# Optimization experiments

Hardware: AMD Instinct MI355X
Metric: run time of the kernel (lower is better)

The kernel has to match this reference:

```python
import jax, jax.numpy as jnp
import numpy as np

B, N, D = 8, 2048, 1024
NEG = -1e9


def setup_inputs() -> dict:
    key = jax.random.key(0)
    kx, kl, kq, kk, kv, ko = jax.random.split(key, 6)
    x = jax.random.normal(kx, (B, N, D), dtype=jnp.float32)
    # prefix padding mask: each clip has a random valid length in [N//2, N]
    lengths = jax.random.randint(kl, (B,), N // 2, N + 1)
    mask = jnp.arange(N)[None, :] < lengths[:, None]  # [B, N] bool
    s = 1.0 / np.sqrt(D)
    Wq = jax.random.normal(kq, (D, D), dtype=jnp.float32) * s  # nn.Linear weight [out,in]
    Wk = jax.random.normal(kk, (D, D), dtype=jnp.float32) * s
    Wv = jax.random.normal(kv, (D, D), dtype=jnp.float32) * s
    Wo = jax.random.normal(ko, (D, D), dtype=jnp.float32) * s
    return {"x": x, "mask": mask, "Wq": Wq, "Wk": Wk, "Wv": Wv, "Wo": Wo}


def reference(x, mask, Wq, Wk, Wv, Wo):
    # Linear (no bias): y = x @ W.T
    K = jnp.einsum('bnd,ed->bne', x, Wk)
    Q = jnp.einsum('bnd,ed->bne', x, Wq) * 0.06
    V = jnp.einsum('bnd,ed->bne', x, Wv)
    logits = jnp.einsum('bne,bme->bnm', Q, K)  # [B, N, N]
    # attention_mask = outer product of padding mask (matmul of mask with its transpose)
    attn_mask = mask[:, :, None] & mask[:, None, :]
    logits = jnp.where(attn_mask, logits, NEG)
    att_weights = jax.nn.softmax(logits, axis=-1)
    # dropout (p=0.5) is identity in eval mode
    # y = (V^T @ W)^T  ->  y[b,i,:] = sum_j att[b,j,i] * V[b,j,:]
    y = jnp.einsum('bji,bjd->bid', att_weights, V)
    y = jnp.einsum('bid,ed->bie', y, Wo)
    return (y, att_weights)
```

## Files before the change

kernel.cpp:

```cpp
#include <hip/hip_runtime.h>
#include <math.h>

typedef __attribute__((ext_vector_type(8))) short short8;
typedef __attribute__((ext_vector_type(4))) float f32x4;

namespace {
constexpr int B_ = 8;
constexpr int N_ = 2048;
constexpr int D_ = 1024;
constexpr float NEGV = -1.0e9f;
}

__device__ __forceinline__ unsigned short f2bf(float x) {
    union { float f; unsigned u; } v; v.f = x;
    unsigned u = v.u + 0x7fffu + ((v.u >> 16) & 1u);
    return (unsigned short)(u >> 16);
}

__global__ __launch_bounds__(256)
void k_lengths(const unsigned char* __restrict__ mask, int* __restrict__ L)
{
    const int b = blockIdx.x;
    const int t = threadIdx.x;
    const bool u8 = (mask[1] != 0);
    int cnt = 0;
    if (u8) {
        for (int n = t; n < N_; n += 256)
            cnt += (mask[(size_t)b * N_ + n] != 0) ? 1 : 0;
    } else {
        const int* mi = (const int*)mask;
        for (int n = t; n < N_; n += 256)
            cnt += (mi[(size_t)b * N_ + n] != 0) ? 1 : 0;
    }
    __shared__ int red[256];
    red[t] = cnt;
    __syncthreads();
    for (int s = 128; s > 0; s >>= 1) {
        if (t < s) red[t] += red[t + s];
        __syncthreads();
    }
    if (t == 0) L[b] = red[0];
}

__global__ __launch_bounds__(256)
void convert_bf16(const float* __restrict__ in, unsigned short* __restrict__ out,
                  int n4, float alpha)
{
    const int i = blockIdx.x * 256 + threadIdx.x;
    if (i >= n4) return;
    const float4 v = ((const float4*)in)[i];
    ushort4 o;
    o.x = f2bf(v.x * alpha); o.y = f2bf(v.y * alpha);
    o.z = f2bf(v.z * alpha); o.w = f2bf(v.w * alpha);
    ((ushort4*)out)[i] = o;
}

template <int OUT_MODE>
__global__ __launch_bounds__(512, 2)
void gemm_nt_256(const unsigned short* __restrict__ A, int lda, long strideA,
                 const unsigned short* __restrict__ Bm, int ldb, long strideB,
                 void* __restrict__ Cout, int ldc, long strideC,
                 int K, const int* __restrict__ Lp)
{
    __shared__ __attribute__((aligned(16))) short As[2][8192];
    __shared__ __attribute__((aligned(16))) short Bs[2][8192];

    const int tid  = threadIdx.x;
    const int lane = tid & 63;
    const int wave = tid >> 6;
    const int wr   = wave >> 2;
    const int wc   = wave & 3;

    const unsigned gx   = gridDim.x;
    const unsigned gxy  = gx * gridDim.y;
    const unsigned total = gxy * gridDim.z;
    const unsigned orig = blockIdx.x + gx * blockIdx.y + gxy * blockIdx.z;
    unsigned wg = orig;
    if ((total & 7u) == 0u)
        wg = (orig & 7u) * (total >> 3) + (orig >> 3);
    const unsigned bz  = wg / gxy;
    const unsigned rem = wg - bz * gxy;
    const unsigned byy = rem / gx;
    const unsigned bxx = rem - byy * gx;

    const int b  = (int)bz;
    const int m0 = (int)byy * 256;
    const int n0 = (int)bxx * 256;

    int Lb = 0;
    if (OUT_MODE == 2) {
        Lb = Lp[b];
        if (m0 >= Lb) return;
        if (n0 >= Lb) {
            float* C = (float*)Cout + (long)b * strideC;
            const float4 nv = make_float4(NEGV, NEGV, NEGV, NEGV);
            const int rl = tid >> 6;
            const int c4 = (tid & 63) * 4;
#pragma unroll
            for (int l = 0; l < 32; ++l)
                *(float4*)(C + (long)(m0 + l * 8 + rl) * ldc + n0 + c4) = nv;
            return;
        }
    }

    const unsigned short* Ab = A  + (long)b * strideA;
    const unsigned short* Bb = Bm + (long)b * strideB;

    const int srow = tid >> 2;
    const int sseg = ((tid & 3) ^ ((tid >> 3) & 3)) * 8;
    const unsigned short* gA = Ab + (long)(m0 + srow) * lda + sseg;
    const unsigned short* gB = Bb + (long)(n0 + srow) * ldb + sseg;
    const int ldst = (tid & ~63) * 8;

    const int q  = lane >> 4, r = lane & 15;
    const int arb = (wr * 128 + r) * 32;
    const int brb = (wc * 64 + r) * 32;
    const int pk  = (q ^ ((r >> 1) & 3)) * 8;

    const int NT = K >> 5;

    short8 aQ[8];
    short8 bQ[4];
    f32x4  acc[8][4] = {};

#define STAGE_A(dd, kt) do {                                                   \
    __builtin_amdgcn_global_load_lds(                                          \
        (const __attribute__((address_space(1))) void*)(gA + (long)(kt)*32),   \
        (__attribute__((address_space(3))) void*)(&As[dd][ldst]), 16, 0, 0);   \
    __builtin_amdgcn_global_load_lds(                                          \
        (const __attribute__((address_space(1))) void*)(gA + (long)128*lda + (long)(kt)*32), \
        (__attribute__((address_space(3))) void*)(&As[dd][4096 + ldst]), 16, 0, 0);          \
} while (0)

#define STAGE_B(dd, kt) do {                                                   \
    __builtin_amdgcn_global_load_lds(                                          \
        (const __attribute__((address_space(1))) void*)(gB + (long)(kt)*32),   \
        (__attribute__((address_space(3))) void*)(&Bs[dd][ldst]), 16, 0, 0);   \
    __builtin_amdgcn_global_load_lds(                                          \
        (const __attribute__((address_space(1))) void*)(gB + (long)128*ldb + (long)(kt)*32), \
        (__attribute__((address_space(3))) void*)(&Bs[dd][4096 + ldst]), 16, 0, 0);          \
} while (0)

#define RD_A(dd) do {                                                          \
    _Pragma("unroll") for (int mr_ = 0; mr_ < 8; ++mr_)                        \
        aQ[mr_] = *(const short8*)&As[dd][arb + mr_ * 512 + pk];               \
} while (0)

#define RD_B(dd, nh) do {                                                      \
    bQ[(nh)*2 + 0] = *(const short8*)&Bs[dd][brb + ((nh)*2 + 0) * 512 + pk];   \
    bQ[(nh)*2 + 1] = *(const short8*)&Bs[dd][brb + ((nh)*2 + 1) * 512 + pk];   \
} while (0)

#define BARX __builtin_amdgcn_s_barrier()
#define WAIT_LGKM0 do { asm volatile("s_waitcnt lgkmcnt(0)" ::: "memory"); \
                        __builtin_amdgcn_sched_barrier(0); } while (0)
#define WAIT_VM0   do { asm volatile("s_waitcnt vmcnt(0)"   ::: "memory"); \
                        __builtin_amdgcn_sched_barrier(0); } while (0)
#define WAIT_VM2   do { asm volatile("s_waitcnt vmcnt(2)"   ::: "memory"); \
                        __builtin_amdgcn_sched_barrier(0); } while (0)

#define MFMA_PH(nh) do {                                                       \
    __builtin_amdgcn_s_setprio(1);                                             \
    _Pragma("unroll") for (int mr_ = 0; mr_ < 8; ++mr_)                        \
    _Pragma("unroll") for (int nr_ = 0; nr_ < 2; ++nr_)                        \
        acc[mr_][(nh)*2 + nr_] = __builtin_amdgcn_mfma_f32_16x16x32_bf16(      \
            aQ[mr_], bQ[(nh)*2 + nr_], acc[mr_][(nh)*2 + nr_], 0, 0, 0);       \
    __builtin_amdgcn_s_setprio(0);                                             \
} while (0)

#define TILE_STEP(d, kt) do {                                                  \
                                                                       \
    RD_A(d); RD_B(d, 0);                                                       \
    if ((kt) + 1 < NT) STAGE_B((d) ^ 1, (kt) + 1);                             \
    BARX; WAIT_LGKM0; MFMA_PH(0); BARX;                                        \
                                                                       \
    RD_B(d, 1);                                                                \
    if ((kt) + 2 < NT) { STAGE_A(d, (kt) + 2); WAIT_VM2; } else { WAIT_VM0; }  \
    BARX; WAIT_LGKM0; MFMA_PH(1); BARX;                                        \
} while (0)

    STAGE_A(0, 0); STAGE_B(0, 0); STAGE_A(1, 1);
    WAIT_VM2; BARX;

    for (int kt = 0; kt < NT; kt += 2) {
        TILE_STEP(0, kt);
        TILE_STEP(1, kt + 1);
    }

#undef STAGE_A
#undef STAGE_B
#undef RD_A
#undef RD_B
#undef BARX
#undef WAIT_LGKM0
#undef WAIT_VM0
#undef WAIT_VM2
#undef MFMA_PH
#undef TILE_STEP

    const int rbase = m0 + wr * 128;
    const int cbase = n0 + wc * 64;
    if (OUT_MODE == 1) {
        unsigned short* C = (unsigned short*)Cout + (long)b * strideC;
#pragma unroll
        for (int mt = 0; mt < 8; ++mt)
#pragma unroll
            for (int nt = 0; nt < 4; ++nt)
#pragma unroll
                for (int rr = 0; rr < 4; ++rr) {
                    const int grow = rbase + mt * 16 + q * 4 + rr;
                    const int gcol = cbase + nt * 16 + r;
                    C[(long)grow * ldc + gcol] = f2bf(acc[mt][nt][rr]);
                }
    } else if (OUT_MODE == 0) {
        float* C = (float*)Cout + (long)b * strideC;
#pragma unroll
        for (int mt = 0; mt < 8; ++mt)
#pragma unroll
            for (int nt = 0; nt < 4; ++nt)
#pragma unroll
                for (int rr = 0; rr < 4; ++rr) {
                    const int grow = rbase + mt * 16 + q * 4 + rr;
                    const int gcol = cbase + nt * 16 + r;
                    C[(long)grow * ldc + gcol] = acc[mt][nt][rr];
                }
    } else {
        float* C = (float*)Cout + (long)b * strideC;
#pragma unroll
        for (int mt = 0; mt < 8; ++mt)
#pragma unroll
            for (int nt = 0; nt < 4; ++nt)
#pragma unroll
                for (int rr = 0; rr < 4; ++rr) {
                    const int grow = rbase + mt * 16 + q * 4 + rr;
                    const int gcol = cbase + nt * 16 + r;
                    const float val = (grow < Lb && gcol < Lb) ? acc[mt][nt][rr] : NEGV;
                    C[(long)grow * ldc + gcol] = val;
                }
    }
}

__global__ __launch_bounds__(256)
void softmax_rows(float* __restrict__ Att, const int* __restrict__ Lp)
{
    const size_t row = blockIdx.x;
    const int i = (int)(row & (N_ - 1));
    const int b = (int)(row >> 11);
    float* p = Att + row * (size_t)N_;
    const int t = threadIdx.x;

    if (i >= Lp[b]) {
        const float c = 1.0f / 2048.0f;
        const float4 cv = make_float4(c, c, c, c);
        *(float4*)(p + t * 4)        = cv;
        *(float4*)(p + 1024 + t * 4) = cv;
        return;
    }

    float4 v0 = *(float4*)(p + t * 4);
    float4 v1 = *(float4*)(p + 1024 + t * 4);

    float mx = fmaxf(fmaxf(fmaxf(v0.x, v0.y), fmaxf(v0.z, v0.w)),
                     fmaxf(fmaxf(v1.x, v1.y), fmaxf(v1.z, v1.w)));
#pragma unroll
    for (int o = 32; o > 0; o >>= 1) mx = fmaxf(mx, __shfl_xor(mx, o, 64));

    __shared__ float red[8];
    const int wv = t >> 6;
    if ((t & 63) == 0) red[wv] = mx;
    __syncthreads();
    mx = fmaxf(fmaxf(red[0], red[1]), fmaxf(red[2], red[3]));

    float e[8];
    e[0] = expf(v0.x - mx); e[1] = expf(v0.y - mx);
    e[2] = expf(v0.z - mx); e[3] = expf(v0.w - mx);
    e[4] = expf(v1.x - mx); e[5] = expf(v1.y - mx);
    e[6] = expf(v1.z - mx); e[7] = expf(v1.w - mx);
    float s = ((e[0] + e[1]) + (e[2] + e[3])) + ((e[4] + e[5]) + (e[6] + e[7]));
#pragma unroll
    for (int o = 32; o > 0; o >>= 1) s += __shfl_xor(s, o, 64);
    if ((t & 63) == 0) red[4 + wv] = s;
    __syncthreads();
    const float inv = 1.0f / (red[4] + red[5] + red[6] + red[7]);

    *(float4*)(p + t * 4)        = make_float4(e[0] * inv, e[1] * inv, e[2] * inv, e[3] * inv);
    *(float4*)(p + 1024 + t * 4) = make_float4(e[4] * inv, e[5] * inv, e[6] * inv, e[7] * inv);
}

__global__ __launch_bounds__(256)
void transpose_att_bf16(const float* __restrict__ att, unsigned short* __restrict__ attT)
{
    __shared__ float tile[64][65];
    const int b  = blockIdx.z;
    const int j0 = blockIdx.y * 64;
    const int i0 = blockIdx.x * 64;
    const float* src = att + (long)b * N_ * N_;
    unsigned short* dst = attT + (long)b * N_ * N_;
    const int t = threadIdx.x;
#pragma unroll
    for (int l = 0; l < 4; ++l) {
        const int idx = t + l * 256;
        const int jj = idx >> 4;
        const int i4 = (idx & 15) * 4;
        const float4 v = *(const float4*)(src + (long)(j0 + jj) * N_ + i0 + i4);
        tile[i4 + 0][jj] = v.x;
        tile[i4 + 1][jj] = v.y;
        tile[i4 + 2][jj] = v.z;
        tile[i4 + 3][jj] = v.w;
    }
    __syncthreads();
#pragma unroll
    for (int l = 0; l < 4; ++l) {
        const int idx = t + l * 256;
        const int ii = idx >> 4;
        const int j4 = (idx & 15) * 4;
        ushort4 o;
        o.x = f2bf(tile[ii][j4 + 0]);
        o.y = f2bf(tile[ii][j4 + 1]);
        o.z = f2bf(tile[ii][j4 + 2]);
        o.w = f2bf(tile[ii][j4 + 3]);
        *(ushort4*)(dst + (long)(i0 + ii) * N_ + j0 + j4) = o;
    }
}

__global__ __launch_bounds__(256)
void transpose_v_bf16(const unsigned short* __restrict__ qkv, unsigned short* __restrict__ vt)
{
    __shared__ unsigned short tile[64][68];
    const int j0 = blockIdx.x * 64;
    const int d0 = blockIdx.y * 64;
    const int t = threadIdx.x;
#pragma unroll
    for (int l = 0; l < 4; ++l) {
        const int idx = t + l * 256;
        const int jj = idx >> 4;
        const int d4 = (idx & 15) * 4;
        const ushort4 v = *(const ushort4*)(qkv + (long)(j0 + jj) * 3072 + 2048 + d0 + d4);
        tile[d4 + 0][jj] = v.x;
        tile[d4 + 1][jj] = v.y;
        tile[d4 + 2][jj] = v.z;
        tile[d4 + 3][jj] = v.w;
    }
    __syncthreads();
#pragma unroll
    for (int l = 0; l < 4; ++l) {
        const int idx = t + l * 256;
        const int dd = idx >> 4;
        const int j4 = (idx & 15) * 4;
        ushort4 o;
        o.x = tile[dd][j4 + 0];
        o.y = tile[dd][j4 + 1];
        o.z = tile[dd][j4 + 2];
        o.w = tile[dd][j4 + 3];
        *(ushort4*)(vt + (long)(d0 + dd) * 16384 + j0 + j4) = o;
    }
}

extern "C" void kernel_launch(void* const* d_in, const int* in_sizes, int n_in,
                              void* d_out, int out_size, void* d_ws, size_t ws_size,
                              hipStream_t stream)
{
    const float* x  = (const float*)d_in[0];
    const unsigned char* mask = (const unsigned char*)d_in[1];
    const float* Wq = (const float*)d_in[2];
    const float* Wk = (const float*)d_in[3];
    const float* Wv = (const float*)d_in[4];
    const float* Wo = (const float*)d_in[5];

    float* y   = (float*)d_out;
    float* att = (float*)d_out + (size_t)B_ * N_ * D_;

    char* ws = (char*)d_ws;
    int* L = (int*)ws;
    unsigned short* Wqkvb = (unsigned short*)(ws + 256);
    unsigned short* Wob   = Wqkvb + 3145728;
    unsigned short* xb    = Wob + 1048576;
    unsigned short* QKVb  = xb + 16777216;
    unsigned short* VT    = QKVb + 50331648;
    unsigned short* attT  = QKVb;
    unsigned short* ctx   = xb;

    const dim3 blk(256);
    const dim3 blk512(512);
    const long NN = (long)N_ * N_;
    const long ND = (long)N_ * D_;
    const long NQ = (long)N_ * 3072;

    k_lengths<<<dim3(B_), blk, 0, stream>>>(mask, L);

    convert_bf16<<<dim3(16384), blk, 0, stream>>>(x,  xb,  4194304, 1.0f);
    convert_bf16<<<dim3(1024),  blk, 0, stream>>>(Wq, Wqkvb,           262144, 0.06f);
    convert_bf16<<<dim3(1024),  blk, 0, stream>>>(Wk, Wqkvb + 1048576, 262144, 1.0f);
    convert_bf16<<<dim3(1024),  blk, 0, stream>>>(Wv, Wqkvb + 2097152, 262144, 1.0f);
    convert_bf16<<<dim3(1024),  blk, 0, stream>>>(Wo, Wob,             262144, 1.0f);

    gemm_nt_256<1><<<dim3(12, 64, 1), blk512, 0, stream>>>(
        xb, D_, 0, Wqkvb, D_, 0, QKVb, 3072, 0, D_, nullptr);

    transpose_v_bf16<<<dim3(256, 16), blk, 0, stream>>>(QKVb, VT);

    gemm_nt_256<2><<<dim3(8, 8, B_), blk512, 0, stream>>>(
        QKVb, 3072, NQ, QKVb + 1024, 3072, NQ, att, N_, NN, D_, L);

    softmax_rows<<<dim3(B_ * N_), blk, 0, stream>>>(att, L);

    transpose_att_bf16<<<dim3(32, 32, B_), blk, 0, stream>>>(att, attT);

    gemm_nt_256<1><<<dim3(4, 8, B_), blk512, 0, stream>>>(
        attT, N_, NN, VT, B_ * N_, N_, ctx, D_, ND, N_, nullptr);

    gemm_nt_256<0><<<dim3(4, 64, 1), blk512, 0, stream>>>(
        ctx, D_, 0, Wob, D_, 0, y, D_, 0, D_, nullptr);
}
```

Baseline: 633.3 us.

## Deepen GEMM LDS pipeline to four stages and split MFMA by M halves

The bf16 NT GEMM kernel moves from a two-buffer LDS scheme to a four-buffer ring that prefetches three K-tiles ahead, with vmcnt waits adjusted to match. The inner step now reads all four B fragments up front and half of A at a time, issuing MFMAs in two M halves instead of two N halves. This is meant to hide global-load latency better and cut A register pressure. In exchange LDS use doubles to 128 KB per block, which may prevent two blocks of 512 threads from co-residing on a CU as the launch bounds request.

```diff
diff --git a/kernel.cpp b/kernel.cpp
--- a/kernel.cpp
+++ b/kernel.cpp
@@ -62,8 +62,8 @@
                  void* __restrict__ Cout, int ldc, long strideC,
                  int K, const int* __restrict__ Lp)
 {
-    __shared__ __attribute__((aligned(16))) short As[2][8192];
-    __shared__ __attribute__((aligned(16))) short Bs[2][8192];
+    __shared__ __attribute__((aligned(16))) short As[4][8192];
+    __shared__ __attribute__((aligned(16))) short Bs[4][8192];
 
     const int tid  = threadIdx.x;
     const int lane = tid & 63;
@@ -119,7 +119,7 @@
 
     const int NT = K >> 5;
 
-    short8 aQ[8];
+    short8 aH[4];
     short8 bQ[4];
     f32x4  acc[8][4] = {};
 
@@ -141,14 +141,14 @@
         (__attribute__((address_space(3))) void*)(&Bs[dd][4096 + ldst]), 16, 0, 0);          \
 } while (0)
 
-#define RD_A(dd) do {                                                          \
-    _Pragma("unroll") for (int mr_ = 0; mr_ < 8; ++mr_)                        \
-        aQ[mr_] = *(const short8*)&As[dd][arb + mr_ * 512 + pk];               \
+#define RD_A_H(dd, mh) do {                                                    \
+    _Pragma("unroll") for (int mr_ = 0; mr_ < 4; ++mr_)                        \
+        aH[mr_] = *(const short8*)&As[dd][arb + ((mh)*4 + mr_) * 512 + pk];    \
 } while (0)
 
-#define RD_B(dd, nh) do {                                                      \
-    bQ[(nh)*2 + 0] = *(const short8*)&Bs[dd][brb + ((nh)*2 + 0) * 512 + pk];   \
-    bQ[(nh)*2 + 1] = *(const short8*)&Bs[dd][brb + ((nh)*2 + 1) * 512 + pk];   \
+#define RD_B_ALL(dd) do {                                                      \
+    _Pragma("unroll") for (int nr_ = 0; nr_ < 4; ++nr_)                        \
+        bQ[nr_] = *(const short8*)&Bs[dd][brb + nr_ * 512 + pk];               \
 } while (0)
 
 #define BARX __builtin_amdgcn_s_barrier()
@@ -156,47 +156,48 @@
                         __builtin_amdgcn_sched_barrier(0); } while (0)
 #define WAIT_VM0   do { asm volatile("s_waitcnt vmcnt(0)"   ::: "memory"); \
                         __builtin_amdgcn_sched_barrier(0); } while (0)
-#define WAIT_VM2   do { asm volatile("s_waitcnt vmcnt(2)"   ::: "memory"); \
+#define WAIT_VM4   do { asm volatile("s_waitcnt vmcnt(4)"   ::: "memory"); \
                         __builtin_amdgcn_sched_barrier(0); } while (0)
-
-#define MFMA_PH(nh) do {                                                       \
+#define WAIT_VM8   do { asm volatile("s_waitcnt vmcnt(8)"   ::: "memory"); \
+                        __builtin_amdgcn_sched_barrier(0); } while (0)
+
+#define MFMA_H(mh) do {                                                        \
     __builtin_amdgcn_s_setprio(1);                                             \
-    _Pragma("unroll") for (int mr_ = 0; mr_ < 8; ++mr_)                        \
-    _Pragma("unroll") for (int nr_ = 0; nr_ < 2; ++nr_)                        \
-        acc[mr_][(nh)*2 + nr_] = __builtin_amdgcn_mfma_f32_16x16x32_bf16(      \
-            aQ[mr_], bQ[(nh)*2 + nr_], acc[mr_][(nh)*2 + nr_], 0, 0, 0);       \
+    _Pragma("unroll") for (int mr_ = 0; mr_ < 4; ++mr_)                        \
+    _Pragma("unroll") for (int nr_ = 0; nr_ < 4; ++nr_)                        \
+        acc[(mh)*4 + mr_][nr_] = __builtin_amdgcn_mfma_f32_16x16x32_bf16(      \
+            aH[mr_], bQ[nr_], acc[(mh)*4 + mr_][nr_], 0, 0, 0);                \
     __builtin_amdgcn_s_setprio(0);                                             \
 } while (0)
 
-#define TILE_STEP(d, kt) do {                                                  \
-                                                                       \
-    RD_A(d); RD_B(d, 0);                                                       \
-    if ((kt) + 1 < NT) STAGE_B((d) ^ 1, (kt) + 1);                             \
-    BARX; WAIT_LGKM0; MFMA_PH(0); BARX;                                        \
-                                                                       \
-    RD_B(d, 1);                                                                \
-    if ((kt) + 2 < NT) { STAGE_A(d, (kt) + 2); WAIT_VM2; } else { WAIT_VM0; }  \
-    BARX; WAIT_LGKM0; MFMA_PH(1); BARX;                                        \
-} while (0)
-
-    STAGE_A(0, 0); STAGE_B(0, 0); STAGE_A(1, 1);
-    WAIT_VM2; BARX;
-
-    for (int kt = 0; kt < NT; kt += 2) {
-        TILE_STEP(0, kt);
-        TILE_STEP(1, kt + 1);
+    STAGE_B(0, 0); STAGE_A(0, 0);
+    STAGE_B(1, 1); STAGE_A(1, 1);
+    STAGE_B(2, 2); STAGE_A(2, 2);
+    WAIT_VM8; BARX;
+
+    for (int kt = 0; kt < NT; ++kt) {
+        const int d  = kt & 3;
+        const int dn = (kt + 3) & 3;
+        RD_A_H(d, 0); RD_B_ALL(d);
+        if (kt + 3 < NT) STAGE_B(dn, kt + 3);
+        BARX; WAIT_LGKM0; MFMA_H(0); BARX;
+        RD_A_H(d, 1);
+        if (kt + 3 < NT) { STAGE_A(dn, kt + 3); WAIT_VM8; }
+        else if (kt + 2 < NT) { WAIT_VM4; }
+        else { WAIT_VM0; }
+        BARX; WAIT_LGKM0; MFMA_H(1); BARX;
     }
 
 #undef STAGE_A
 #undef STAGE_B
-#undef RD_A
-#undef RD_B
+#undef RD_A_H
+#undef RD_B_ALL
 #undef BARX
 #undef WAIT_LGKM0
 #undef WAIT_VM0
-#undef WAIT_VM2
-#undef MFMA_PH
-#undef TILE_STEP
+#undef WAIT_VM4
+#undef WAIT_VM8
+#undef MFMA_H
 
     const int rbase = m0 + wr * 128;
     const int cbase = n0 + wc * 64;
```

After: 619.4 us. 2.2% less time.
